# Optimization experiments

Hardware: AMD Instinct MI355X
Metric: run time of the kernel (lower is better)

Reference implementation:

```python
import jax, jax.numpy as jnp
import numpy as np

D, H, HD, F, A, P, NB, MD = 1024, 16, 64, 2816, 64, 30, 32, 128
B, L = 4, 1024


def _rel_bucket(rel, num_buckets=NB, max_distance=MD):
    # T5 relative position bucket, bidirectional=False (decoder self-attn)
    rel = -jnp.minimum(rel, 0)
    max_exact = num_buckets // 2
    is_small = rel < max_exact
    large = max_exact + (
        jnp.log(jnp.maximum(rel, 1).astype(jnp.float32) / max_exact)
        / np.log(max_distance / max_exact)
        * (num_buckets - max_exact)
    ).astype(jnp.int32)
    large = jnp.minimum(large, num_buckets - 1)
    return jnp.where(is_small, rel, large)


def _rmsnorm(x, scale, eps=1e-6):
    var = jnp.mean(jnp.square(x), axis=-1, keepdims=True)
    return x * jax.lax.rsqrt(var + eps) * scale


def _attn(x, kv, wq, wk, wv, wo, mask, bias, pk, pv):
    # x: [B,Lq,D], kv: [B,Lk,D], prefix pk/pv: [B,P,H,HD]
    hd = wq.shape[-1]
    q = jnp.einsum('bqd,dhe->bqhe', x, wq) * (hd ** -0.5)
    k = jnp.einsum('bkd,dhe->bkhe', kv, wk)
    v = jnp.einsum('bkd,dhe->bkhe', kv, wv)
    k = jnp.concatenate([pk, k], axis=1)  # prefix KV prepended
    v = jnp.concatenate([pv, v], axis=1)
    logits = jnp.einsum('bqhe,bkhe->bhqk', q, k).astype(jnp.float32)
    p = pk.shape[1]
    if bias is not None:
        logits = logits + jnp.pad(bias, ((0, 0), (0, 0), (0, 0), (p, 0)))
    mask = jnp.pad(mask, ((0, 0), (0, 0), (0, 0), (p, 0)), constant_values=True)
    logits = jnp.where(mask, logits, jnp.float32(-1e10))
    w = jax.nn.softmax(logits, axis=-1).astype(x.dtype)
    o = jnp.einsum('bhqk,bkhe->bqhe', w, v)
    return jnp.einsum('bqhe,hed->bqd', o, wo)


def setup_inputs() -> dict:
    key = jax.random.key(0)
    ks = jax.random.split(key, 24)
    s = D ** -0.5
    inp = {
        'inputs': jax.random.normal(ks[0], (B, L, D), jnp.float32),
        'encoded': jax.random.normal(ks[1], (B, L, D), jnp.float32),
        'adapter_wd': jax.random.normal(ks[2], (B, D, A), jnp.float32) * s,
        'adapter_wu': jax.random.normal(ks[3], (B, A, D), jnp.float32) * (A ** -0.5),
        'adapter_bd': jax.random.normal(ks[4], (B, A), jnp.float32) * 0.02,
        'adapter_bu': jax.random.normal(ks[5], (B, D), jnp.float32) * 0.02,
        'prefix_key': jax.random.normal(ks[6], (B, 2, P, H, HD), jnp.float32),
        'prefix_value': jax.random.normal(ks[7], (B, 2, P, H, HD), jnp.float32),
        'ln1': jnp.ones((D,), jnp.float32),
        'ln2': jnp.ones((D,), jnp.float32),
        'ln3': jnp.ones((D,), jnp.float32),
        'sa_wq': jax.random.normal(ks[8], (D, H, HD), jnp.float32) * s,
        'sa_wk': jax.random.normal(ks[9], (D, H, HD), jnp.float32) * s,
        'sa_wv': jax.random.normal(ks[10], (D, H, HD), jnp.float32) * s,
        'sa_wo': jax.random.normal(ks[11], (H, HD, D), jnp.float32) * s,
        'ca_wq': jax.random.normal(ks[12], (D, H, HD), jnp.float32) * s,
        'ca_wk': jax.random.normal(ks[13], (D, H, HD), jnp.float32) * s,
        'ca_wv': jax.random.normal(ks[14], (D, H, HD), jnp.float32) * s,
        'ca_wo': jax.random.normal(ks[15], (H, HD, D), jnp.float32) * s,
        'relpos': jax.random.normal(ks[16], (H, NB), jnp.float32) * 0.1,
        'mlp_wi0': jax.random.normal(ks[17], (D, F), jnp.float32) * s,
        'mlp_wi1': jax.random.normal(ks[18], (D, F), jnp.float32) * s,
        'mlp_wo': jax.random.normal(ks[19], (F, D), jnp.float32) * (F ** -0.5),
        'decoder_mask': jnp.broadcast_to(jnp.tril(jnp.ones((L, L), bool))[None, None], (B, 1, L, L)),
        'encoder_decoder_mask': jnp.ones((B, 1, L, L), bool),
    }
    return inp


def reference(inputs, encoded, adapter_wd, adapter_wu, adapter_bd, adapter_bu,
              prefix_key, prefix_value, ln1, ln2, ln3,
              sa_wq, sa_wk, sa_wv, sa_wo, ca_wq, ca_wk, ca_wv, ca_wo,
              relpos, mlp_wi0, mlp_wi1, mlp_wo,
              decoder_mask, encoder_decoder_mask):
    l = inputs.shape[1]
    pos = jnp.arange(l)
    buckets = _rel_bucket(pos[None, :] - pos[:, None])  # [L,L]
    bias = relpos[:, buckets][None]                      # [1,H,L,L]
    # self-attention with prefix + relative bias
    x = _rmsnorm(inputs, ln1)
    x = _attn(x, x, sa_wq, sa_wk, sa_wv, sa_wo, decoder_mask, bias,
              prefix_key[:, 0], prefix_value[:, 0])
    x = x + inputs
    # cross-attention with prefix
    y = _rmsnorm(x, ln2)
    y = _attn(y, encoded, ca_wq, ca_wk, ca_wv, ca_wo, encoder_decoder_mask, None,
              prefix_key[:, 1], prefix_value[:, 1])
    y = y + x
    # gated-gelu MLP + per-example adapter
    lz = _rmsnorm(y, ln3)
    z = (jax.nn.gelu(lz @ mlp_wi0) * (lz @ mlp_wi1)) @ mlp_wo
    az = jnp.einsum('bld,bda->bla', lz, adapter_wd) + adapter_bd[:, None]
    az = jax.nn.gelu(az)
    az = jnp.einsum('bla,bad->bld', az, adapter_wu) + adapter_bu[:, None]
    z = z + az
    return z + y
```

## Files before the change

kernel.cpp:

```cpp
#include <hip/hip_runtime.h>

typedef unsigned short u16;
typedef __attribute__((ext_vector_type(8))) __bf16 bf16x8;
typedef __attribute__((ext_vector_type(4))) float f32x4;

__device__ __forceinline__ float bf2f(u16 u) {
  union { unsigned int i; float f; } v; v.i = ((unsigned int)u) << 16; return v.f;
}
__device__ __forceinline__ u16 f2bf(float f) {
  unsigned int x = __float_as_uint(f);
  unsigned int r = (x + 0x7fffu + ((x >> 16) & 1u)) >> 16;
  return (u16)r;
}
__device__ __forceinline__ u16 f2bf_fast(float f) {
  return (u16)((__float_as_uint(f) + 0x8000u) >> 16);
}
__device__ __forceinline__ float gelu_f(float x) {
  float u = 0.7978845608028654f * (x + 0.044715f * x * x * x);
  float t = 1.0f - 2.0f / (__expf(2.0f * u) + 1.0f);
  return 0.5f * x * (1.0f + t);
}
__device__ __forceinline__ void gl_lds16(const u16* g, u16* l) {
  __builtin_amdgcn_global_load_lds(
      (const __attribute__((address_space(1))) unsigned int*)g,
      (__attribute__((address_space(3))) unsigned int*)l, 16, 0, 0);
}

__global__ __launch_bounds__(256) void cast_bf16_k(const float* __restrict__ in,
                                                   u16* __restrict__ out, int n4) {
  int i = blockIdx.x * 256 + threadIdx.x;
  if (i >= n4) return;
  float4 v = ((const float4*)in)[i];
  ushort4 o;
  o.x = f2bf(v.x); o.y = f2bf(v.y); o.z = f2bf(v.z); o.w = f2bf(v.w);
  ((ushort4*)out)[i] = o;
}

__global__ __launch_bounds__(256) void transpose_k(
    const float* __restrict__ in, u16* __restrict__ out, int R, int C,
    long isb, long osb) {
  __shared__ u16 tile[32][33];
  in += (size_t)blockIdx.z * isb;
  out += (size_t)blockIdx.z * osb;
  int c0 = blockIdx.x * 32, r0 = blockIdx.y * 32;
  int tx = threadIdx.x & 31, ty = threadIdx.x >> 5;
#pragma unroll
  for (int i = 0; i < 4; ++i) {
    int rr = r0 + ty + i * 8;
    if (rr < R && c0 + tx < C) tile[ty + i * 8][tx] = f2bf(in[(size_t)rr * C + c0 + tx]);
  }
  __syncthreads();
#pragma unroll
  for (int i = 0; i < 4; ++i) {
    int cc = c0 + ty + i * 8;
    if (cc < C && r0 + tx < R) out[(size_t)cc * R + r0 + tx] = tile[tx][ty + i * 8];
  }
}

__global__ __launch_bounds__(256) void bias_tab_k(const float* __restrict__ relpos,
                                                  float* __restrict__ tab) {
  int idx = blockIdx.x * 256 + threadIdx.x;
  int h = idx >> 10, d = idx & 1023;
  int bucket;
  if (d < 16) bucket = d;
  else {
    int lb = 16 + (int)(logf((float)d * (1.0f / 16.0f)) * (16.0f / logf(8.0f)));
    bucket = lb < 31 ? lb : 31;
  }
  tab[idx] = relpos[h * 32 + bucket];
}

__global__ __launch_bounds__(256) void prefix_fill_k(
    const float* __restrict__ pK, const float* __restrict__ pV,
    u16* __restrict__ Kd, u16* __restrict__ Vtd, int sSel) {
  int idx = blockIdx.x * 256 + threadIdx.x;
  int e = idx & 63, p = (idx >> 6) & 31, h = (idx >> 11) & 15, b = idx >> 15;
  int key = (p < 30) ? p : (1024 + p);
  float kv = 0.f, vv = 0.f;
  if (p < 30) {
    size_t src = ((((size_t)(b * 2 + sSel)) * 30 + p) * 16 + h) * 64 + e;
    kv = pK[src]; vv = pV[src];
  }
  Kd[(((size_t)(b * 16 + h)) * 1056 + key) * 64 + e] = f2bf(kv);
  Vtd[(((size_t)(b * 16 + h)) * 64 + e) * 1056 + key] = f2bf(vv);
}

__global__ __launch_bounds__(256) void rmsnorm_k(const float* __restrict__ in,
                                                 const float* __restrict__ scale,
                                                 u16* __restrict__ out) {
  const int D = 1024;
  size_t base = (size_t)blockIdx.x * D;
  int t = threadIdx.x;
  float x[4];
#pragma unroll
  for (int i = 0; i < 4; ++i) x[i] = in[base + t + i * 256];
  float s = x[0] * x[0] + x[1] * x[1] + x[2] * x[2] + x[3] * x[3];
#pragma unroll
  for (int off = 1; off < 64; off <<= 1) s += __shfl_xor(s, off, 64);
  __shared__ float ws4[4];
  if ((t & 63) == 0) ws4[t >> 6] = s;
  __syncthreads();
  float tot = ws4[0] + ws4[1] + ws4[2] + ws4[3];
  float r = rsqrtf(tot * (1.0f / D) + 1e-6f);
#pragma unroll
  for (int i = 0; i < 4; ++i) {
    int c = t + i * 256;
    out[base + c] = f2bf(x[i] * r * scale[c]);
  }
}

__global__ __launch_bounds__(256) void gelumul_k(const u16* __restrict__ g2,
                                                 u16* __restrict__ g) {
  int i = blockIdx.x * 256 + threadIdx.x;
  int m = i / 352, f8 = i - m * 352;
  size_t b0 = (size_t)m * 5632 + f8 * 8;
  uint4 h0 = *(const uint4*)(g2 + b0);
  uint4 h1 = *(const uint4*)(g2 + b0 + 2816);
  const u16* p0 = (const u16*)&h0;
  const u16* p1 = (const u16*)&h1;
  uint4 ov;
  u16* po = (u16*)&ov;
#pragma unroll
  for (int j = 0; j < 8; ++j) po[j] = f2bf(gelu_f(bf2f(p0[j])) * bf2f(p1[j]));
  *(uint4*)(g + (size_t)m * 2816 + f8 * 8) = ov;
}

template <int MODE>
__global__ __launch_bounds__(256) void gemm97(
    const u16* __restrict__ A, const u16* __restrict__ Bt, void* __restrict__ out,
    void* __restrict__ out2, void* __restrict__ out3,
    const float* __restrict__ res1, int M, int N, int K, int Ks, float alpha) {
  const int BK = 32;
  __shared__ __align__(16) u16 As[128 * 32];
  __shared__ __align__(16) u16 Bs[128 * 32];

  const int t = threadIdx.x;
  const int wave = t >> 6, lane = t & 63;
  int wgid = blockIdx.y * gridDim.x + blockIdx.x;
  const int cpx = (gridDim.x * gridDim.y) >> 3;
  wgid = (wgid & 7) * cpx + (wgid >> 3);
  const int m0 = (wgid / gridDim.x) * 128, n0 = (wgid % gridDim.x) * 128;
  const int kbase = blockIdx.z * Ks;
  const int fr = lane & 15, fq = lane >> 4;
  const int wm = (wave >> 1) * 64, wn = (wave & 1) * 64;

  const int srow = wave * 32 + (lane >> 2);
  const int scol = (lane & 3) * 8;
  const u16* ag0 = A + (size_t)(m0 + srow) * K + kbase + scol;
  const u16* ag1 = ag0 + (size_t)16 * K;
  const u16* bg0 = Bt + (size_t)(n0 + srow) * K + kbase + scol;
  const u16* bg1 = bg0 + (size_t)16 * K;
  u16* al0 = &As[(wave * 32) * 32];
  u16* al1 = &As[(wave * 32 + 16) * 32];
  u16* bl0 = &Bs[(wave * 32) * 32];
  u16* bl1 = &Bs[(wave * 32 + 16) * 32];

  f32x4 acc[16];
#pragma unroll
  for (int i = 0; i < 16; ++i) acc[i] = (f32x4){0.f, 0.f, 0.f, 0.f};

  for (int k0 = 0; k0 < Ks; k0 += BK) {
    gl_lds16(ag0 + k0, al0);
    gl_lds16(ag1 + k0, al1);
    gl_lds16(bg0 + k0, bl0);
    gl_lds16(bg1 + k0, bl1);
    __syncthreads();
    bf16x8 af[4], bf[4];
#pragma unroll
    for (int i = 0; i < 4; ++i)
      af[i] = *(const bf16x8*)&As[(wm + i * 16 + fr) * 32 + fq * 8];
#pragma unroll
    for (int j = 0; j < 4; ++j)
      bf[j] = *(const bf16x8*)&Bs[(wn + j * 16 + fr) * 32 + fq * 8];
#pragma unroll
    for (int i = 0; i < 4; ++i)
#pragma unroll
      for (int j = 0; j < 4; ++j)
        acc[i * 4 + j] = __builtin_amdgcn_mfma_f32_16x16x32_bf16(
            af[i], bf[j], acc[i * 4 + j], 0, 0, 0);
    __syncthreads();
  }

#pragma unroll
  for (int i = 0; i < 4; ++i) {
#pragma unroll
    for (int rr = 0; rr < 4; ++rr) {
      long gm = (long)m0 + wm + i * 16 + fq * 4 + rr;
#pragma unroll
      for (int j = 0; j < 4; ++j) {
        int gn = n0 + wn + j * 16 + fr;
        float v = acc[i * 4 + j][rr];
        size_t oi = (size_t)gm * N + gn;
        if (MODE == 0) ((float*)out)[oi] = v;
        if (MODE == 1) {
          float* po = blockIdx.z ? (float*)out2 : (float*)out;
          po[oi] = v;
        }
        if (MODE == 2) ((u16*)out)[oi] = f2bf(v);
        if (MODE == 3) ((float*)out)[oi] = v + res1[oi];
        if (MODE == 8) {
          int b = (int)(gm >> 10), l = (int)(gm & 1023), h = gn >> 6, e = gn & 63;
          ((u16*)out)[(((size_t)(b * 16 + h)) * 1024 + l) * 64 + e] = f2bf(v * alpha);
        }
        if (MODE == 11) {
          int b = (int)(gm >> 10), l = (int)(gm & 1023);
          int sec = gn >> 10, nn = gn & 1023, h = nn >> 6, e = nn & 63;
          if (sec == 0)
            ((u16*)out)[(((size_t)(b * 16 + h)) * 1024 + l) * 64 + e] = f2bf(v * alpha);
          else if (sec == 1)
            ((u16*)out2)[(((size_t)(b * 16 + h)) * 1056 + 30 + l) * 64 + e] = f2bf(v);
          else
            ((u16*)out3)[(((size_t)(b * 16 + h)) * 64 + e) * 1056 + 30 + l] = f2bf(v);
        }
        if (MODE == 12) {
          int b = (int)(gm >> 10), l = (int)(gm & 1023);
          int sec = gn >> 10, nn = gn & 1023, h = nn >> 6, e = nn & 63;
          if (sec == 0)
            ((u16*)out)[(((size_t)(b * 16 + h)) * 1056 + 30 + l) * 64 + e] = f2bf(v);
          else
            ((u16*)out2)[(((size_t)(b * 16 + h)) * 64 + e) * 1056 + 30 + l] = f2bf(v);
        }
      }
    }
  }
}

template <int MODE>
__global__ __launch_bounds__(256) void gemm_bt(
    const u16* __restrict__ A, const u16* __restrict__ Bt, void* __restrict__ out,
    const float* __restrict__ res1, const float* __restrict__ res2,
    const float* __restrict__ res3, const float* __restrict__ bias,
    int M, int N, int K,
    long Asb, long Bsb, long bsb, long r1sb, long r2sb, long r3sb, long osb) {
  const int BM = 128, BK = 32, LP = 40;
  __shared__ __align__(16) u16 As[BM * LP];
  __shared__ __align__(16) u16 Bs[BM * LP];

  const int t = threadIdx.x;
  const int m0 = blockIdx.y * BM;
  const int n0 = blockIdx.x * 128;
  const int bz = blockIdx.z;
  A += (size_t)bz * Asb;
  Bt += (size_t)bz * Bsb;

  f32x4 acc[16];
#pragma unroll
  for (int i = 0; i < 16; ++i) acc[i] = (f32x4){0.f, 0.f, 0.f, 0.f};
  const int wave = t >> 6, lane = t & 63;
  const int wm = (wave >> 1) * 64, wn = (wave & 1) * 64;
  const int fr = lane & 15, fq = lane >> 4;

  for (int k0 = 0; k0 < K; k0 += BK) {
#pragma unroll
    for (int i = 0; i < 2; ++i) {
      int idx = (i * 256 + t) * 8;
      int row = idx >> 5, col = idx & 31;
      *(uint4*)&As[row * LP + col] =
          *(const uint4*)(A + (size_t)(m0 + row) * K + k0 + col);
      uint4 bv = {0u, 0u, 0u, 0u};
      if (n0 + row < N) bv = *(const uint4*)(Bt + (size_t)(n0 + row) * K + k0 + col);
      *(uint4*)&Bs[row * LP + col] = bv;
    }
    __syncthreads();
    bf16x8 af[4], bfr[4];
#pragma unroll
    for (int i = 0; i < 4; ++i)
      af[i] = *(const bf16x8*)&As[(wm + i * 16 + fr) * LP + fq * 8];
#pragma unroll
    for (int j = 0; j < 4; ++j)
      bfr[j] = *(const bf16x8*)&Bs[(wn + j * 16 + fr) * LP + fq * 8];
#pragma unroll
    for (int i = 0; i < 4; ++i)
#pragma unroll
      for (int j = 0; j < 4; ++j)
        acc[i * 4 + j] = __builtin_amdgcn_mfma_f32_16x16x32_bf16(
            af[i], bfr[j], acc[i * 4 + j], 0, 0, 0);
    __syncthreads();
  }

#pragma unroll
  for (int i = 0; i < 4; ++i) {
#pragma unroll
    for (int rr = 0; rr < 4; ++rr) {
      long gm = (long)m0 + wm + i * 16 + fq * 4 + rr;
#pragma unroll
      for (int j = 0; j < 4; ++j) {
        int gn = n0 + wn + j * 16 + fr;
        if (gn >= N) continue;
        float v = acc[i * 4 + j][rr];
        size_t oi = (size_t)bz * osb + (size_t)gm * N + gn;
        size_t ri = (size_t)gm * N + gn;
        if (MODE == 6) ((u16*)out)[oi] = f2bf(gelu_f(v + bias[(size_t)bz * bsb + gn]));
        if (MODE == 7)
          ((float*)out)[oi] = v + bias[(size_t)bz * bsb + gn] +
                              res1[(size_t)bz * r1sb + ri] +
                              res2[(size_t)bz * r2sb + ri] +
                              res3[(size_t)bz * r3sb + ri];
      }
    }
  }
}

template <bool IS_SELF>
__global__ __launch_bounds__(256) void fattn_k(
    const u16* __restrict__ Qg, const u16* __restrict__ Kg,
    const u16* __restrict__ Vtg, const float* __restrict__ bias_tab,
    u16* __restrict__ Out) {
  const int L = 1024, P = 30, KC = 1056;
  const int flat = blockIdx.x;
  const int wg = (flat & 7) * 64 + (flat >> 3);
  const int q0b = (wg & 7) * 128;
  const int h = (wg >> 3) & 15, b = wg >> 7;
  const int t = threadIdx.x, wave = t >> 6, lane = t & 63;
  const int fr = lane & 15, fq = lane >> 4;
  const int q0w = q0b + wave * 32;

  __shared__ float bTs[IS_SELF ? 1024 : 4];
  __shared__ __align__(16) u16 Ps[4][32][40];

  if (IS_SELF) {
#pragma unroll
    for (int i = 0; i < 4; ++i) bTs[t + i * 256] = bias_tab[h * 1024 + t + i * 256];
    __syncthreads();
  }

  const u16* qptr = Qg + (((size_t)(b * 16 + h)) * L + q0w + fr) * 64 + fq * 8;
  bf16x8 qa0 = *(const bf16x8*)qptr;
  bf16x8 qa1 = *(const bf16x8*)(qptr + 32);
  bf16x8 qb0 = *(const bf16x8*)(qptr + 16 * 64);
  bf16x8 qb1 = *(const bf16x8*)(qptr + 16 * 64 + 32);

  f32x4 oA[4], oB[4];
#pragma unroll
  for (int i = 0; i < 4; ++i) {
    oA[i] = (f32x4){0.f, 0.f, 0.f, 0.f};
    oB[i] = (f32x4){0.f, 0.f, 0.f, 0.f};
  }
  f32x4 olA = (f32x4){0.f, 0.f, 0.f, 0.f};
  f32x4 olB = (f32x4){0.f, 0.f, 0.f, 0.f};
  bf16x8 ones;
  {
    u16 one = 0x3F80;
#pragma unroll
    for (int i = 0; i < 8; ++i) ((u16*)&ones)[i] = one;
  }

  const int nk = IS_SELF ? (P + q0b + 128) : (P + L);
  const int nch = (nk + 31) >> 5;
  const u16* kp = Kg + ((size_t)(b * 16 + h)) * KC * 64 + (size_t)fr * 64 + fq * 8;
  const u16* vp = Vtg + ((size_t)(b * 16 + h)) * 64 * KC + (size_t)fr * KC + fq * 8;

  bf16x8 kf0 = *(const bf16x8*)(kp + 0);
  bf16x8 kf1 = *(const bf16x8*)(kp + 32);
  bf16x8 kf2 = *(const bf16x8*)(kp + 16 * 64);
  bf16x8 kf3 = *(const bf16x8*)(kp + 16 * 64 + 32);

  auto smax = [&](f32x4* s, int k0, int qoff, int rb) {
    const bool full = IS_SELF ? (k0 >= 32 && k0 + 31 - P <= qoff)
                              : (k0 + 31 < P + L);
    if (full) {
      if (IS_SELF) {
#pragma unroll
        for (int reg = 0; reg < 4; ++reg) {
          const int qq = qoff + fq * 4 + reg;
          s[0][reg] += bTs[qq - (k0 + fr - P)];
          s[1][reg] += bTs[qq - (k0 + 16 + fr - P)];
        }
      }
    } else {
#pragma unroll
      for (int reg = 0; reg < 4; ++reg) {
        const int qq = qoff + fq * 4 + reg;
#pragma unroll
        for (int t2 = 0; t2 < 2; ++t2) {
          const int kvi = k0 + t2 * 16 + fr;
          float sv = s[t2][reg];
          if (IS_SELF) {
            const int lk = kvi - P;
            if (lk >= 0) {
              if (lk <= qq) sv += bTs[qq - lk];
              else sv = -3.0e38f;
            }
          } else {
            if (kvi >= P + L) sv = -3.0e38f;
          }
          s[t2][reg] = sv;
        }
      }
    }
#pragma unroll
    for (int reg = 0; reg < 4; ++reg) {
      Ps[wave][rb + fq * 4 + reg][fr] = f2bf_fast(__expf(s[0][reg]));
      Ps[wave][rb + fq * 4 + reg][16 + fr] = f2bf_fast(__expf(s[1][reg]));
    }
  };

  for (int ch = 0; ch < nch; ++ch) {
    const int k0 = ch * 32;
    bf16x8 vf0 = *(const bf16x8*)(vp + 0 * 16 * KC + k0);
    bf16x8 vf1 = *(const bf16x8*)(vp + 1 * 16 * KC + k0);
    bf16x8 vf2 = *(const bf16x8*)(vp + 2 * 16 * KC + k0);
    bf16x8 vf3 = *(const bf16x8*)(vp + 3 * 16 * KC + k0);
    const int k0n = (ch + 1 < nch) ? (k0 + 32) : 0;
    bf16x8 kn0 = *(const bf16x8*)(kp + (size_t)k0n * 64);
    bf16x8 kn1 = *(const bf16x8*)(kp + (size_t)k0n * 64 + 32);
    bf16x8 kn2 = *(const bf16x8*)(kp + (size_t)(k0n + 16) * 64);
    bf16x8 kn3 = *(const bf16x8*)(kp + (size_t)(k0n + 16) * 64 + 32);

    f32x4 sA[2], sB[2];
    sA[0] = (f32x4){0.f, 0.f, 0.f, 0.f};
    sA[1] = (f32x4){0.f, 0.f, 0.f, 0.f};
    sB[0] = (f32x4){0.f, 0.f, 0.f, 0.f};
    sB[1] = (f32x4){0.f, 0.f, 0.f, 0.f};
    sA[0] = __builtin_amdgcn_mfma_f32_16x16x32_bf16(qa0, kf0, sA[0], 0, 0, 0);
    sA[0] = __builtin_amdgcn_mfma_f32_16x16x32_bf16(qa1, kf1, sA[0], 0, 0, 0);
    sA[1] = __builtin_amdgcn_mfma_f32_16x16x32_bf16(qa0, kf2, sA[1], 0, 0, 0);
    sA[1] = __builtin_amdgcn_mfma_f32_16x16x32_bf16(qa1, kf3, sA[1], 0, 0, 0);
    sB[0] = __builtin_amdgcn_mfma_f32_16x16x32_bf16(qb0, kf0, sB[0], 0, 0, 0);
    sB[0] = __builtin_amdgcn_mfma_f32_16x16x32_bf16(qb1, kf1, sB[0], 0, 0, 0);
    sB[1] = __builtin_amdgcn_mfma_f32_16x16x32_bf16(qb0, kf2, sB[1], 0, 0, 0);
    sB[1] = __builtin_amdgcn_mfma_f32_16x16x32_bf16(qb1, kf3, sB[1], 0, 0, 0);

    smax(sA, k0, q0w, 0);
    smax(sB, k0, q0w + 16, 16);
    __asm__ volatile("s_waitcnt lgkmcnt(0)" ::: "memory");
    bf16x8 paA = *(const bf16x8*)&Ps[wave][fr][fq * 8];
    bf16x8 paB = *(const bf16x8*)&Ps[wave][16 + fr][fq * 8];

    oA[0] = __builtin_amdgcn_mfma_f32_16x16x32_bf16(paA, vf0, oA[0], 0, 0, 0);
    oA[1] = __builtin_amdgcn_mfma_f32_16x16x32_bf16(paA, vf1, oA[1], 0, 0, 0);
    oA[2] = __builtin_amdgcn_mfma_f32_16x16x32_bf16(paA, vf2, oA[2], 0, 0, 0);
    oA[3] = __builtin_amdgcn_mfma_f32_16x16x32_bf16(paA, vf3, oA[3], 0, 0, 0);
    olA   = __builtin_amdgcn_mfma_f32_16x16x32_bf16(paA, ones, olA, 0, 0, 0);
    oB[0] = __builtin_amdgcn_mfma_f32_16x16x32_bf16(paB, vf0, oB[0], 0, 0, 0);
    oB[1] = __builtin_amdgcn_mfma_f32_16x16x32_bf16(paB, vf1, oB[1], 0, 0, 0);
    oB[2] = __builtin_amdgcn_mfma_f32_16x16x32_bf16(paB, vf2, oB[2], 0, 0, 0);
    oB[3] = __builtin_amdgcn_mfma_f32_16x16x32_bf16(paB, vf3, oB[3], 0, 0, 0);
    olB   = __builtin_amdgcn_mfma_f32_16x16x32_bf16(paB, ones, olB, 0, 0, 0);

    kf0 = kn0; kf1 = kn1; kf2 = kn2; kf3 = kn3;
  }

  float invA[4], invB[4];
#pragma unroll
  for (int reg = 0; reg < 4; ++reg) {
    invA[reg] = 1.0f / olA[reg];
    invB[reg] = 1.0f / olB[reg];
  }
#pragma unroll
  for (int dt = 0; dt < 4; ++dt) {
#pragma unroll
    for (int reg = 0; reg < 4; ++reg) {
      size_t rowA = (size_t)(b * L + q0w + fq * 4 + reg);
      Out[(rowA * 16 + h) * 64 + dt * 16 + fr] = f2bf(oA[dt][reg] * invA[reg]);
      size_t rowB = rowA + 16;
      Out[(rowB * 16 + h) * 64 + dt * 16 + fr] = f2bf(oB[dt][reg] * invB[reg]);
    }
  }
}

extern "C" void kernel_launch(void* const* d_in, const int* in_sizes, int n_in,
                              void* d_out, int out_size, void* d_ws, size_t ws_size,
                              hipStream_t stream) {
  const int B = 4, L = 1024, D = 1024, H = 16, F = 2816, AD = 64;
  const int M = B * L;
  const int KC = 1056;

  const float* inputs  = (const float*)d_in[0];
  const float* encoded = (const float*)d_in[1];
  const float* a_wd    = (const float*)d_in[2];
  const float* a_wu    = (const float*)d_in[3];
  const float* a_bd    = (const float*)d_in[4];
  const float* a_bu    = (const float*)d_in[5];
  const float* pK      = (const float*)d_in[6];
  const float* pV      = (const float*)d_in[7];
  const float* ln1     = (const float*)d_in[8];
  const float* ln2     = (const float*)d_in[9];
  const float* ln3     = (const float*)d_in[10];
  const float* sa_wq   = (const float*)d_in[11];
  const float* sa_wk   = (const float*)d_in[12];
  const float* sa_wv   = (const float*)d_in[13];
  const float* sa_wo   = (const float*)d_in[14];
  const float* ca_wq   = (const float*)d_in[15];
  const float* ca_wk   = (const float*)d_in[16];
  const float* ca_wv   = (const float*)d_in[17];
  const float* ca_wo   = (const float*)d_in[18];
  const float* relpos  = (const float*)d_in[19];
  const float* wi0     = (const float*)d_in[20];
  const float* wi1     = (const float*)d_in[21];
  const float* wom     = (const float*)d_in[22];

  char* w = (char*)d_ws;
  size_t used = 0;
  auto alloc = [&](size_t bytes) {
    char* p = w + used;
    used += (bytes + 255) & ~(size_t)255;
    return p;
  };
  u16* wqkvT  = (u16*)alloc((size_t)3072 * 1024 * 2);
  u16* woT    = (u16*)alloc((size_t)D * 1024 * 2);
  u16* cqT    = (u16*)alloc((size_t)D * 1024 * 2);
  u16* ckvT   = (u16*)alloc((size_t)2048 * 1024 * 2);
  u16* coT    = (u16*)alloc((size_t)D * 1024 * 2);
  u16* wi01T  = (u16*)alloc((size_t)5632 * 1024 * 2);
  u16* womT   = (u16*)alloc((size_t)D * F * 2);
  u16* wdT    = (u16*)alloc((size_t)B * AD * D * 2);
  u16* wuT    = (u16*)alloc((size_t)B * D * AD * 2);
  float* bT   = (float*)alloc((size_t)H * 1024 * 4);
  u16* enc16  = (u16*)alloc((size_t)M * D * 2);
  u16* xn     = (u16*)alloc((size_t)M * D * 2);
  u16* lz     = (u16*)alloc((size_t)M * D * 2);
  u16* Kc     = (u16*)alloc((size_t)B * H * KC * 64 * 2);
  u16* Vtc    = (u16*)alloc((size_t)B * H * 64 * KC * 2);
  u16* qh     = (u16*)alloc((size_t)B * H * L * 64 * 2);
  u16* ao     = (u16*)alloc((size_t)M * D * 2);
  float* xf   = (float*)alloc((size_t)M * D * 4);
  float* yf   = (float*)alloc((size_t)M * D * 4);
  u16* az1    = (u16*)alloc((size_t)B * 1024 * AD * 2);
  u16* g2     = Kc;
  u16* g      = enc16;
  float* zf0  = (float*)Kc;
  float* zf1  = (float*)Kc + (size_t)M * D;
  if (used > ws_size) return;

  dim3 tb(256);
  auto T = [&](const float* src, u16* dst, int R, int C, int nb, long sb) {
    transpose_k<<<dim3((C + 31) / 32, (R + 31) / 32, nb), tb, 0, stream>>>(
        src, dst, R, C, sb, sb);
  };
  T(sa_wq, wqkvT, D, 1024, 1, 0);
  T(sa_wk, wqkvT + (size_t)1024 * 1024, D, 1024, 1, 0);
  T(sa_wv, wqkvT + (size_t)2048 * 1024, D, 1024, 1, 0);
  T(sa_wo, woT, 1024, D, 1, 0);
  T(ca_wq, cqT, D, 1024, 1, 0);
  T(ca_wk, ckvT, D, 1024, 1, 0);
  T(ca_wv, ckvT + (size_t)1024 * 1024, D, 1024, 1, 0);
  T(ca_wo, coT, 1024, D, 1, 0);
  T(wi0, wi01T, D, F, 1, 0);
  T(wi1, wi01T + (size_t)2816 * 1024, D, F, 1, 0);
  T(wom, womT, F, D, 1, 0);
  T(a_wd, wdT, D, AD, B, (long)D * AD);
  T(a_wu, wuT, AD, D, B, (long)AD * D);
  bias_tab_k<<<dim3(64), tb, 0, stream>>>(relpos, bT);
  cast_bf16_k<<<dim3(M * D / 4 / 256), tb, 0, stream>>>(encoded, enc16, M * D / 4);

#define G97(MODE, Ap, Btp, Op, O2, O3, R1, Nn, Kk, al)                         \
  gemm97<MODE><<<dim3((Nn) / 128, M / 128), tb, 0, stream>>>(                  \
      (const u16*)(Ap), (const u16*)(Btp), (void*)(Op), (void*)(O2),           \
      (void*)(O3), (const float*)(R1), M, Nn, Kk, Kk, al)

  rmsnorm_k<<<dim3(M), tb, 0, stream>>>(inputs, ln1, xn);
  G97(11, xn, wqkvT, qh, Kc, Vtc, nullptr, 3072, D, 0.125f);
  prefix_fill_k<<<dim3(512), tb, 0, stream>>>(pK, pV, Kc, Vtc, 0);
  fattn_k<true><<<dim3(512), tb, 0, stream>>>(qh, Kc, Vtc, bT, ao);
  G97(3, ao, woT, xf, nullptr, nullptr, inputs, 1024, D, 1.f);
  rmsnorm_k<<<dim3(M), tb, 0, stream>>>(xf, ln2, xn);
  G97(8, xn, cqT, qh, nullptr, nullptr, nullptr, 1024, D, 0.125f);
  G97(12, enc16, ckvT, Kc, Vtc, nullptr, nullptr, 2048, D, 1.f);
  prefix_fill_k<<<dim3(512), tb, 0, stream>>>(pK, pV, Kc, Vtc, 1);
  fattn_k<false><<<dim3(512), tb, 0, stream>>>(qh, Kc, Vtc, nullptr, ao);
  G97(3, ao, coT, yf, nullptr, nullptr, xf, 1024, D, 1.f);
  rmsnorm_k<<<dim3(M), tb, 0, stream>>>(yf, ln3, lz);
  gemm_bt<6><<<dim3(1, 8, B), tb, 0, stream>>>(
      lz, wdT, az1, nullptr, nullptr, nullptr, a_bd, 1024, AD, D,
      (long)1024 * D, (long)AD * D, (long)AD, 0, 0, 0, (long)1024 * AD);
  G97(2, lz, wi01T, g2, nullptr, nullptr, nullptr, 5632, D, 1.f);
  gelumul_k<<<dim3(5632), tb, 0, stream>>>(g2, g);
  gemm97<1><<<dim3(8, M / 128, 2), tb, 0, stream>>>(
      (const u16*)g, (const u16*)womT, (void*)zf0, (void*)zf1, nullptr,
      nullptr, M, 1024, 2816, 1408, 1.f);
  gemm_bt<7><<<dim3(8, 8, B), tb, 0, stream>>>(
      az1, wuT, d_out, zf0, zf1, yf, a_bu, 1024, 1024, AD,
      (long)1024 * AD, (long)D * AD, (long)1024, (long)1024 * 1024,
      (long)1024 * 1024, (long)1024 * 1024, (long)1024 * 1024);
#undef G97
  (void)in_sizes; (void)n_in; (void)out_size;
}
```

Measured before the change: 718.0 us.

## Fuse gated-GELU into interleaved wi0/wi1 GEMM and split-K output projections

```diff
diff --git a/kernel.cpp b/kernel.cpp
--- a/kernel.cpp
+++ b/kernel.cpp
@@ -38,7 +38,7 @@
 
 __global__ __launch_bounds__(256) void transpose_k(
     const float* __restrict__ in, u16* __restrict__ out, int R, int C,
-    long isb, long osb) {
+    long isb, long osb, int rs, int roff) {
   __shared__ u16 tile[32][33];
   in += (size_t)blockIdx.z * isb;
   out += (size_t)blockIdx.z * osb;
@@ -53,7 +53,8 @@
 #pragma unroll
   for (int i = 0; i < 4; ++i) {
     int cc = c0 + ty + i * 8;
-    if (cc < C && r0 + tx < R) out[(size_t)cc * R + r0 + tx] = tile[tx][ty + i * 8];
+    if (cc < C && r0 + tx < R)
+      out[(size_t)(cc * rs + roff) * R + r0 + tx] = tile[tx][ty + i * 8];
   }
 }
 
@@ -109,20 +110,33 @@
   }
 }
 
-__global__ __launch_bounds__(256) void gelumul_k(const u16* __restrict__ g2,
-                                                 u16* __restrict__ g) {
-  int i = blockIdx.x * 256 + threadIdx.x;
-  int m = i / 352, f8 = i - m * 352;
-  size_t b0 = (size_t)m * 5632 + f8 * 8;
-  uint4 h0 = *(const uint4*)(g2 + b0);
-  uint4 h1 = *(const uint4*)(g2 + b0 + 2816);
-  const u16* p0 = (const u16*)&h0;
-  const u16* p1 = (const u16*)&h1;
-  uint4 ov;
-  u16* po = (u16*)&ov;
-#pragma unroll
-  for (int j = 0; j < 8; ++j) po[j] = f2bf(gelu_f(bf2f(p0[j])) * bf2f(p1[j]));
-  *(uint4*)(g + (size_t)m * 2816 + f8 * 8) = ov;
+__global__ __launch_bounds__(256) void rmsnorm_sum_k(
+    const float* __restrict__ in0, const float* __restrict__ in1,
+    const float* __restrict__ res, const float* __restrict__ scale,
+    u16* __restrict__ outn, float* __restrict__ outs) {
+  const int D = 1024;
+  size_t base = (size_t)blockIdx.x * D;
+  int t = threadIdx.x;
+  float x[4];
+#pragma unroll
+  for (int i = 0; i < 4; ++i) {
+    int c = t + i * 256;
+    x[i] = in0[base + c] + in1[base + c] + res[base + c];
+    outs[base + c] = x[i];
+  }
+  float s = x[0] * x[0] + x[1] * x[1] + x[2] * x[2] + x[3] * x[3];
+#pragma unroll
+  for (int off = 1; off < 64; off <<= 1) s += __shfl_xor(s, off, 64);
+  __shared__ float ws4[4];
+  if ((t & 63) == 0) ws4[t >> 6] = s;
+  __syncthreads();
+  float tot = ws4[0] + ws4[1] + ws4[2] + ws4[3];
+  float r = rsqrtf(tot * (1.0f / D) + 1e-6f);
+#pragma unroll
+  for (int i = 0; i < 4; ++i) {
+    int c = t + i * 256;
+    outn[base + c] = f2bf(x[i] * r * scale[c]);
+  }
 }
 
 template <int MODE>
@@ -136,10 +150,17 @@
 
   const int t = threadIdx.x;
   const int wave = t >> 6, lane = t & 63;
-  int wgid = blockIdx.y * gridDim.x + blockIdx.x;
-  const int cpx = (gridDim.x * gridDim.y) >> 3;
-  wgid = (wgid & 7) * cpx + (wgid >> 3);
-  const int m0 = (wgid / gridDim.x) * 128, n0 = (wgid % gridDim.x) * 128;
+  int m0, n0;
+  if (MODE != 13) {
+    int wgid = blockIdx.y * gridDim.x + blockIdx.x;
+    const int cpx = (gridDim.x * gridDim.y) >> 3;
+    wgid = (wgid & 7) * cpx + (wgid >> 3);
+    m0 = (wgid / gridDim.x) * 128;
+    n0 = (wgid % gridDim.x) * 128;
+  } else {
+    m0 = blockIdx.y * 128;
+    n0 = blockIdx.x * 128;
+  }
   const int kbase = blockIdx.z * Ks;
   const int fr = lane & 15, fq = lane >> 4;
   const int wm = (wave >> 1) * 64, wn = (wave & 1) * 64;
@@ -191,13 +212,11 @@
         int gn = n0 + wn + j * 16 + fr;
         float v = acc[i * 4 + j][rr];
         size_t oi = (size_t)gm * N + gn;
-        if (MODE == 0) ((float*)out)[oi] = v;
         if (MODE == 1) {
           float* po = blockIdx.z ? (float*)out2 : (float*)out;
           po[oi] = v;
         }
         if (MODE == 2) ((u16*)out)[oi] = f2bf(v);
-        if (MODE == 3) ((float*)out)[oi] = v + res1[oi];
         if (MODE == 8) {
           int b = (int)(gm >> 10), l = (int)(gm & 1023), h = gn >> 6, e = gn & 63;
           ((u16*)out)[(((size_t)(b * 16 + h)) * 1024 + l) * 64 + e] = f2bf(v * alpha);
@@ -219,6 +238,11 @@
             ((u16*)out)[(((size_t)(b * 16 + h)) * 1056 + 30 + l) * 64 + e] = f2bf(v);
           else
             ((u16*)out2)[(((size_t)(b * 16 + h)) * 64 + e) * 1056 + 30 + l] = f2bf(v);
+        }
+        if (MODE == 13) {
+          float vo = __shfl_xor(v, 1, 64);
+          if (!(fr & 1))
+            ((u16*)out)[(size_t)gm * 2816 + (gn >> 1)] = f2bf(gelu_f(v) * vo);
         }
       }
     }
@@ -517,30 +541,31 @@
   float* xf   = (float*)alloc((size_t)M * D * 4);
   float* yf   = (float*)alloc((size_t)M * D * 4);
   u16* az1    = (u16*)alloc((size_t)B * 1024 * AD * 2);
-  u16* g2     = Kc;
-  u16* g      = enc16;
-  float* zf0  = (float*)Kc;
-  float* zf1  = (float*)Kc + (size_t)M * D;
+  float* pk0  = (float*)Kc;
+  u16* g      = Kc;
+  float* zf0  = (float*)enc16;
+  float* zf1  = (float*)ao;
   if (used > ws_size) return;
 
   dim3 tb(256);
-  auto T = [&](const float* src, u16* dst, int R, int C, int nb, long sb) {
+  auto T = [&](const float* src, u16* dst, int R, int C, int nb, long sb,
+               int rs, int roff) {
     transpose_k<<<dim3((C + 31) / 32, (R + 31) / 32, nb), tb, 0, stream>>>(
-        src, dst, R, C, sb, sb);
+        src, dst, R, C, sb, sb, rs, roff);
   };
-  T(sa_wq, wqkvT, D, 1024, 1, 0);
-  T(sa_wk, wqkvT + (size_t)1024 * 1024, D, 1024, 1, 0);
-  T(sa_wv, wqkvT + (size_t)2048 * 1024, D, 1024, 1, 0);
-  T(sa_wo, woT, 1024, D, 1, 0);
-  T(ca_wq, cqT, D, 1024, 1, 0);
-  T(ca_wk, ckvT, D, 1024, 1, 0);
-  T(ca_wv, ckvT + (size_t)1024 * 1024, D, 1024, 1, 0);
-  T(ca_wo, coT, 1024, D, 1, 0);
-  T(wi0, wi01T, D, F, 1, 0);
-  T(wi1, wi01T + (size_t)2816 * 1024, D, F, 1, 0);
-  T(wom, womT, F, D, 1, 0);
-  T(a_wd, wdT, D, AD, B, (long)D * AD);
-  T(a_wu, wuT, AD, D, B, (long)AD * D);
+  T(sa_wq, wqkvT, D, 1024, 1, 0, 1, 0);
+  T(sa_wk, wqkvT + (size_t)1024 * 1024, D, 1024, 1, 0, 1, 0);
+  T(sa_wv, wqkvT + (size_t)2048 * 1024, D, 1024, 1, 0, 1, 0);
+  T(sa_wo, woT, 1024, D, 1, 0, 1, 0);
+  T(ca_wq, cqT, D, 1024, 1, 0, 1, 0);
+  T(ca_wk, ckvT, D, 1024, 1, 0, 1, 0);
+  T(ca_wv, ckvT + (size_t)1024 * 1024, D, 1024, 1, 0, 1, 0);
+  T(ca_wo, coT, 1024, D, 1, 0, 1, 0);
+  T(wi0, wi01T, D, F, 1, 0, 2, 0);
+  T(wi1, wi01T, D, F, 1, 0, 2, 1);
+  T(wom, womT, F, D, 1, 0, 1, 0);
+  T(a_wd, wdT, D, AD, B, (long)D * AD, 1, 0);
+  T(a_wu, wuT, AD, D, B, (long)AD * D, 1, 0);
   bias_tab_k<<<dim3(64), tb, 0, stream>>>(relpos, bT);
   cast_bf16_k<<<dim3(M * D / 4 / 256), tb, 0, stream>>>(encoded, enc16, M * D / 4);
 
@@ -553,19 +578,24 @@
   G97(11, xn, wqkvT, qh, Kc, Vtc, nullptr, 3072, D, 0.125f);
   prefix_fill_k<<<dim3(512), tb, 0, stream>>>(pK, pV, Kc, Vtc, 0);
   fattn_k<true><<<dim3(512), tb, 0, stream>>>(qh, Kc, Vtc, bT, ao);
-  G97(3, ao, woT, xf, nullptr, nullptr, inputs, 1024, D, 1.f);
-  rmsnorm_k<<<dim3(M), tb, 0, stream>>>(xf, ln2, xn);
+  gemm97<1><<<dim3(8, M / 128, 2), tb, 0, stream>>>(
+      (const u16*)ao, (const u16*)woT, (void*)pk0, (void*)xf, nullptr,
+      nullptr, M, 1024, 1024, 512, 1.f);
+  rmsnorm_sum_k<<<dim3(M), tb, 0, stream>>>(pk0, xf, inputs, ln2, xn, xf);
   G97(8, xn, cqT, qh, nullptr, nullptr, nullptr, 1024, D, 0.125f);
   G97(12, enc16, ckvT, Kc, Vtc, nullptr, nullptr, 2048, D, 1.f);
   prefix_fill_k<<<dim3(512), tb, 0, stream>>>(pK, pV, Kc, Vtc, 1);
   fattn_k<false><<<dim3(512), tb, 0, stream>>>(qh, Kc, Vtc, nullptr, ao);
-  G97(3, ao, coT, yf, nullptr, nullptr, xf, 1024, D, 1.f);
-  rmsnorm_k<<<dim3(M), tb, 0, stream>>>(yf, ln3, lz);
+  gemm97<1><<<dim3(8, M / 128, 2), tb, 0, stream>>>(
+      (const u16*)ao, (const u16*)coT, (void*)pk0, (void*)yf, nullptr,
+      nullptr, M, 1024, 1024, 512, 1.f);
+  rmsnorm_sum_k<<<dim3(M), tb, 0, stream>>>(pk0, yf, xf, ln3, lz, yf);
   gemm_bt<6><<<dim3(1, 8, B), tb, 0, stream>>>(
       lz, wdT, az1, nullptr, nullptr, nullptr, a_bd, 1024, AD, D,
       (long)1024 * D, (long)AD * D, (long)AD, 0, 0, 0, (long)1024 * AD);
-  G97(2, lz, wi01T, g2, nullptr, nullptr, nullptr, 5632, D, 1.f);
-  gelumul_k<<<dim3(5632), tb, 0, stream>>>(g2, g);
+  gemm97<13><<<dim3(5632 / 128, M / 128), tb, 0, stream>>>(
+      (const u16*)lz, (const u16*)wi01T, (void*)g, nullptr, nullptr,
+      nullptr, M, 5632, 1024, 1024, 1.f);
   gemm97<1><<<dim3(8, M / 128, 2), tb, 0, stream>>>(
       (const u16*)g, (const u16*)womT, (void*)zf0, (void*)zf1, nullptr,
       nullptr, M, 1024, 2816, 1408, 1.f);
```

After: 713.8 us. No clear change (-0.6%).
